# Performance work log

Hardware: AMD Instinct MI355X
Metric: run time of the kernel (lower is better)

Reference implementation:

```python
import jax, jax.numpy as jnp
import numpy as np

EMBED = 1024
D_MODEL = 1024
HEADS = 16
HEAD_DIM = D_MODEL // HEADS


def setup_inputs() -> dict:
    key = jax.random.key(0)
    ks = jax.random.split(key, 9)
    s = 1.0 / np.sqrt(EMBED)
    inp = {
        "x": jax.random.normal(ks[0], (4, 2048, EMBED), dtype=jnp.float32),
        "Wq": jax.random.uniform(ks[1], (EMBED, D_MODEL), jnp.float32, -s, s),
        "bq": jax.random.uniform(ks[2], (D_MODEL,), jnp.float32, -s, s),
        "Wk": jax.random.uniform(ks[3], (EMBED, D_MODEL), jnp.float32, -s, s),
        "bk": jax.random.uniform(ks[4], (D_MODEL,), jnp.float32, -s, s),
        "Wv": jax.random.uniform(ks[5], (EMBED, D_MODEL), jnp.float32, -s, s),
        "bv": jax.random.uniform(ks[6], (D_MODEL,), jnp.float32, -s, s),
        "Wo": jax.random.uniform(ks[7], (D_MODEL, D_MODEL), jnp.float32, -s, s),
        "bo": jax.random.uniform(ks[8], (D_MODEL,), jnp.float32, -s, s),
    }
    return inp


def reference(x, Wq, bq, Wk, bk, Wv, bv, Wo, bo):
    B, S, _ = x.shape
    # projections -> [B, H, S, Dh]
    def proj(W, b):
        return (x @ W + b).reshape(B, S, HEADS, HEAD_DIM).transpose(0, 2, 1, 3)
    q = proj(Wq, bq)
    k = proj(Wk, bk)
    v = proj(Wv, bv)
    energy = jnp.einsum("bhqd,bhkd->bhqk", q, k)  # [B,H,S,S]
    attn = jax.nn.softmax(energy / jnp.sqrt(jnp.float32(HEAD_DIM)), axis=-1)
    out = jnp.einsum("bhqk,bhkd->bhqd", attn, v)
    out = out.transpose(0, 2, 1, 3).reshape(B, S, D_MODEL)
    return out @ Wo + bo
```

## Files before the change

### kernel.cpp

```cpp
#include <hip/hip_runtime.h>

typedef unsigned short u16;
typedef unsigned int u32;
typedef unsigned short u16x8 __attribute__((ext_vector_type(8)));
typedef short s16x4 __attribute__((ext_vector_type(4)));
typedef __bf16 bf16x8 __attribute__((ext_vector_type(8)));
typedef float f32x4 __attribute__((ext_vector_type(4)));

#define QSCALE 0.18033688011112042f

__device__ __forceinline__ u16 f2bf(float f) {
    unsigned u = __float_as_uint(f);
    u += 0x7fffu + ((u >> 16) & 1u);
    return (u16)(u >> 16);
}

__device__ __forceinline__ bf16x8 ldfrag(const u16* p) {
    return __builtin_bit_cast(bf16x8, *(const u16x8*)p);
}

__device__ __forceinline__ void async_cp16(const void* g, void* l) {
    __builtin_amdgcn_global_load_lds(
        (const __attribute__((address_space(1))) unsigned int*)g,
        (__attribute__((address_space(3))) unsigned int*)l, 16, 0, 0);
}

__device__ __forceinline__ uint2 pack4(float a, float b, float c, float d) {
    uint2 w;
    w.x = (u32)f2bf(a) | ((u32)f2bf(b) << 16);
    w.y = (u32)f2bf(c) | ((u32)f2bf(d) << 16);
    return w;
}

__device__ __forceinline__ f32x4 mfma16(uint2 a, uint2 b, f32x4 c) {
#if __has_builtin(__builtin_amdgcn_mfma_f32_16x16x16bf16_1k)
    return __builtin_amdgcn_mfma_f32_16x16x16bf16_1k(
        __builtin_bit_cast(s16x4, a), __builtin_bit_cast(s16x4, b), c, 0, 0, 0);
#else
    asm volatile("s_nop 1\n\tv_mfma_f32_16x16x16_bf16 %0, %1, %2, %0"
                 : "+v"(c) : "v"(a), "v"(b));
    return c;
#endif
}


__global__ void cvt_x(const float* __restrict__ x, u16* __restrict__ xb, int n4) {
    int i = blockIdx.x * blockDim.x + threadIdx.x;
    if (i < n4) {
        float4 v = ((const float4*)x)[i];
        ushort4 o;
        o.x = f2bf(v.x); o.y = f2bf(v.y); o.z = f2bf(v.z); o.w = f2bf(v.w);
        ((ushort4*)xb)[i] = o;
    }
}

__global__ __launch_bounds__(1024) void transp(const float* __restrict__ src, u16* __restrict__ dst) {
    __shared__ float t[32][33];
    int bx = blockIdx.x * 32, by = blockIdx.y * 32;
    t[threadIdx.y][threadIdx.x] = src[(by + threadIdx.y) * 1024 + bx + threadIdx.x];
    __syncthreads();
    dst[(bx + threadIdx.y) * 1024 + by + threadIdx.x] = f2bf(t[threadIdx.x][threadIdx.y]);
}

__global__ void mkbias(const float* __restrict__ bq, const float* __restrict__ bk,
                       const float* __restrict__ bv, float* __restrict__ bqkv) {
    int i = blockIdx.x * blockDim.x + threadIdx.x;
    if (i < 3072) bqkv[i] = (i < 1024) ? bq[i] : (i < 2048 ? bk[i - 1024] : bv[i - 2048]);
}


template <int EPI>
__global__ __launch_bounds__(256)
void gemm128(const u16* __restrict__ A, const u16* __restrict__ Bt,
             const float* __restrict__ bias,
             u16* __restrict__ Qb, u16* __restrict__ Kb, u16* __restrict__ Vt,
             float* __restrict__ outf) {
    __shared__ u16 Asm[128 * 64];
    __shared__ u16 Bsm[128 * 64];
    int tid = threadIdx.x;
    int wave = tid >> 6, lane = tid & 63;
    int lr = lane & 15, lq = lane >> 4;
    int wrow = (wave >> 1) * 64, wcol = (wave & 1) * 64;
    int tileM = blockIdx.y * 128, tileN = blockIdx.x * 128;

    f32x4 acc[4][4];
    for (int i = 0; i < 4; i++)
        for (int j = 0; j < 4; j++)
            acc[i][j] = (f32x4){0.f, 0.f, 0.f, 0.f};

    int srow = tid >> 3;
    int sg = (tid & 7) ^ (srow & 7);
    const u16* ga = A + (tileM + srow) * 1024 + sg * 8;
    const u16* gb = Bt + (tileN + srow) * 1024 + sg * 8;
    u16* la = &Asm[tid * 8];
    u16* lb = &Bsm[tid * 8];

    int sw0 = ((lq ^ (lr & 7)) << 3);
    int sw1 = (((4 + lq) ^ (lr & 7)) << 3);

    for (int k0 = 0; k0 < 1024; k0 += 64) {
        for (int rnd = 0; rnd < 4; rnd++) {
            async_cp16(ga + k0 + rnd * 32 * 1024, la + rnd * 2048);
            async_cp16(gb + k0 + rnd * 32 * 1024, lb + rnd * 2048);
        }
        __syncthreads();
        for (int ko = 0; ko < 2; ko++) {
            int sw = ko ? sw1 : sw0;
            bf16x8 af[4], bfr[4];
            for (int mt = 0; mt < 4; mt++) af[mt] = ldfrag(&Asm[(wrow + mt * 16 + lr) * 64 + sw]);
            for (int nt = 0; nt < 4; nt++) bfr[nt] = ldfrag(&Bsm[(wcol + nt * 16 + lr) * 64 + sw]);
            for (int mt = 0; mt < 4; mt++)
                for (int nt = 0; nt < 4; nt++) {
                    if (EPI == 1)
                        acc[mt][nt] = __builtin_amdgcn_mfma_f32_16x16x32_bf16(af[mt], bfr[nt], acc[mt][nt], 0, 0, 0);
                    else
                        acc[mt][nt] = __builtin_amdgcn_mfma_f32_16x16x32_bf16(bfr[nt], af[mt], acc[mt][nt], 0, 0, 0);
                }
        }
        __syncthreads();
    }

    if (EPI == 0) {
        for (int mt = 0; mt < 4; mt++) {
            int m = tileM + wrow + mt * 16 + lr;
            int b = m >> 11, s = m & 2047;
            for (int nt = 0; nt < 4; nt++) {
                int n0 = tileN + wcol + nt * 16 + lq * 4;
                float4 bn = *(const float4*)&bias[n0];
                int which = n0 >> 10, d = n0 & 1023, h = d >> 6, dh = d & 63;
                u16* dst = (which ? Kb : Qb) + ((b * 16 + h) * 2048 + s) * 64 + dh;
                f32x4 v = acc[mt][nt];
                uint2 w;
                if (which == 0)
                    w = pack4((v[0] + bn.x) * QSCALE, (v[1] + bn.y) * QSCALE,
                              (v[2] + bn.z) * QSCALE, (v[3] + bn.w) * QSCALE);
                else
                    w = pack4(v[0] + bn.x, v[1] + bn.y, v[2] + bn.z, v[3] + bn.w);
                *(uint2*)dst = w;
            }
        }
    } else if (EPI == 1) {
        for (int nt = 0; nt < 4; nt++) {
            int n0 = tileN + wcol + nt * 16 + lr;
            float bn = bias[n0];
            int h = n0 >> 6, dh = n0 & 63;
            for (int mt = 0; mt < 4; mt++) {
                int m0 = tileM + wrow + mt * 16 + lq * 4;
                int b = m0 >> 11, s = m0 & 2047;
                f32x4 v = acc[mt][nt];
                uint2 w = pack4(v[0] + bn, v[1] + bn, v[2] + bn, v[3] + bn);
                *(uint2*)(Vt + ((b * 16 + h) * 64 + dh) * 2048 + s) = w;
            }
        }
    } else {
        for (int mt = 0; mt < 4; mt++) {
            int m = tileM + wrow + mt * 16 + lr;
            for (int nt = 0; nt < 4; nt++) {
                int n0 = tileN + wcol + nt * 16 + lq * 4;
                float4 bn = *(const float4*)&bias[n0];
                f32x4 v = acc[mt][nt];
                float4 st = {v[0] + bn.x, v[1] + bn.y, v[2] + bn.z, v[3] + bn.w};
                *(float4*)&outf[m * 1024 + n0] = st;
            }
        }
    }
}

__global__ __launch_bounds__(256)
void attn(const u16* __restrict__ Qb, const u16* __restrict__ Kb,
          const u16* __restrict__ Vt, u16* __restrict__ Ob) {
    __shared__ u16 Ksm[2][64 * 64];
    __shared__ u16 Vsm[2][64 * 64];
    int tid = threadIdx.x;
    int wave = tid >> 6, lane = tid & 63;
    int lr = lane & 15, lq = lane >> 4;
    int bh = blockIdx.y;
    int b = bh >> 4, h = bh & 15;
    int qbase = blockIdx.x * 128 + wave * 32;

    const u16* Qh = Qb + bh * 2048 * 64;
    const u16* Kh = Kb + bh * 2048 * 64;
    const u16* Vh = Vt + bh * 64 * 2048;

    bf16x8 qf[2][2];
    for (int s = 0; s < 2; s++)
        for (int hf = 0; hf < 2; hf++)
            qf[s][hf] = ldfrag(Qh + (qbase + s * 16 + lr) * 64 + hf * 32 + lq * 8);

    f32x4 o[2][4];
    float lacc[2] = {0.f, 0.f};
    for (int s = 0; s < 2; s++)
        for (int dt = 0; dt < 4; dt++) o[s][dt] = (f32x4){0.f, 0.f, 0.f, 0.f};

    int sw0 = (lq ^ (lr & 7)) << 3;

    int sr = tid >> 3, sg = tid & 7;
    int ksw = ((sg ^ (sr & 7)) << 3);
    const u16* gk = Kh + sr * 64 + ksw;
    const u16* gv = Vh + sr * 2048 + ksw;

    int vsub = (lq & 1) * 4;
    int vx = (lq >> 1);

    async_cp16(gk, &Ksm[0][tid * 8]);
    async_cp16(gk + 32 * 64, &Ksm[0][tid * 8 + 32 * 64]);
    async_cp16(gv, &Vsm[0][tid * 8]);
    async_cp16(gv + 32 * 2048, &Vsm[0][tid * 8 + 32 * 64]);

    for (int it = 0; it < 32; ++it) {
        int p = it & 1;
        __syncthreads();

        if (it < 31) {
            gk += 64 * 64; gv += 64;
            async_cp16(gk, &Ksm[p ^ 1][tid * 8]);
            async_cp16(gk + 32 * 64, &Ksm[p ^ 1][tid * 8 + 32 * 64]);
            async_cp16(gv, &Vsm[p ^ 1][tid * 8]);
            async_cp16(gv + 32 * 2048, &Vsm[p ^ 1][tid * 8 + 32 * 64]);
        }

        uint2 pb[2][4];
        for (int kg = 0; kg < 4; kg++) {
            const u16* krow = &Ksm[p][(kg * 16 + lr) * 64];
            bf16x8 kf0 = ldfrag(krow + sw0);
            bf16x8 kf1 = ldfrag(krow + (sw0 ^ 32));
            for (int s = 0; s < 2; s++) {
                f32x4 a = (f32x4){0.f, 0.f, 0.f, 0.f};
                a = __builtin_amdgcn_mfma_f32_16x16x32_bf16(kf0, qf[s][0], a, 0, 0, 0);
                a = __builtin_amdgcn_mfma_f32_16x16x32_bf16(kf1, qf[s][1], a, 0, 0, 0);
                float e0 = __builtin_amdgcn_exp2f(a[0]);
                float e1 = __builtin_amdgcn_exp2f(a[1]);
                float e2 = __builtin_amdgcn_exp2f(a[2]);
                float e3 = __builtin_amdgcn_exp2f(a[3]);
                lacc[s] += (e0 + e1) + (e2 + e3);
                pb[s][kg] = pack4(e0, e1, e2, e3);
            }
        }

        for (int kg = 0; kg < 4; kg++) {
            int vofs = (((2 * kg + vx) ^ (lr & 7)) << 3) + vsub;
            for (int dt = 0; dt < 4; dt++) {
                uint2 vf = *(const uint2*)&Vsm[p][(dt * 16 + lr) * 64 + vofs];
                o[0][dt] = mfma16(vf, pb[0][kg], o[0][dt]);
                o[1][dt] = mfma16(vf, pb[1][kg], o[1][dt]);
            }
        }
    }

    for (int s = 0; s < 2; s++) {
        lacc[s] += __shfl_xor(lacc[s], 16);
        lacc[s] += __shfl_xor(lacc[s], 32);
    }

    for (int s = 0; s < 2; s++) {
        float linv = 1.0f / lacc[s];
        int q = qbase + s * 16 + lr;
        u16* obase = Ob + (b * 2048 + q) * 1024 + h * 64 + lq * 4;
        for (int dt = 0; dt < 4; dt++) {
            uint2 w = pack4(o[s][dt][0] * linv, o[s][dt][1] * linv,
                            o[s][dt][2] * linv, o[s][dt][3] * linv);
            *(uint2*)(obase + dt * 16) = w;
        }
    }
}


extern "C" void kernel_launch(void* const* d_in, const int* in_sizes, int n_in,
                              void* d_out, int out_size, void* d_ws, size_t ws_size,
                              hipStream_t stream) {
    const float* x  = (const float*)d_in[0];
    const float* Wq = (const float*)d_in[1];
    const float* bq = (const float*)d_in[2];
    const float* Wk = (const float*)d_in[3];
    const float* bk = (const float*)d_in[4];
    const float* Wv = (const float*)d_in[5];
    const float* bv = (const float*)d_in[6];
    const float* Wo = (const float*)d_in[7];
    const float* bo = (const float*)d_in[8];
    float* out = (float*)d_out;

    char* ws = (char*)d_ws;
    u16* xb    = (u16*)ws;
    u16* Wt    = (u16*)(ws + (16u << 20));
    u16* Wot   = (u16*)(ws + (22u << 20));
    float* bqkv = (float*)(ws + (24u << 20));
    u16* Vtb   = (u16*)(ws + (25u << 20));
    u16* Qb    = (u16*)d_out;
    u16* Kb    = Qb + 4 * 16 * 2048 * 64;

    cvt_x<<<8192, 256, 0, stream>>>(x, xb, 8192 * 1024 / 4);
    dim3 tb(32, 32);
    transp<<<dim3(32, 32), tb, 0, stream>>>(Wq, Wt);
    transp<<<dim3(32, 32), tb, 0, stream>>>(Wk, Wt + 1024 * 1024);
    transp<<<dim3(32, 32), tb, 0, stream>>>(Wv, Wt + 2 * 1024 * 1024);
    transp<<<dim3(32, 32), tb, 0, stream>>>(Wo, Wot);
    mkbias<<<12, 256, 0, stream>>>(bq, bk, bv, bqkv);

    gemm128<0><<<dim3(16, 64), 256, 0, stream>>>(xb, Wt, bqkv, Qb, Kb, nullptr, nullptr);
    gemm128<1><<<dim3(8, 64), 256, 0, stream>>>(xb, Wt + 2048 * 1024, bqkv + 2048,
                                                nullptr, nullptr, Vtb, nullptr);
    attn<<<dim3(16, 64), 256, 0, stream>>>(Qb, Kb, Vtb, xb);
    gemm128<2><<<dim3(8, 64), 256, 0, stream>>>(xb, Wot, bo, nullptr, nullptr, nullptr, out);
}
```

Before: 327.7 us.

## Use 16x16x32 MFMA for PV product with permuted K rows and packed bf16 convert

Replaces the 16x16x16 bf16 MFMA used for the P·V product with the wider 16x16x32 instruction. K rows are permuted in shared memory so that each lane's exp'd scores form a contiguous 8-element bf16 fragment usable directly as the B operand. Score packing now uses the hardware v_cvt_pk_bf16_f32 instruction instead of software rounding. The aim is to halve the PV MFMA issue count, use wider LDS reads for V, and cut conversion ALU work, at the cost of a more intricate swizzle that must match between the global-load and read sides.

```diff
diff --git a/kernel.cpp b/kernel.cpp
--- a/kernel.cpp
+++ b/kernel.cpp
@@ -3,7 +3,7 @@
 typedef unsigned short u16;
 typedef unsigned int u32;
 typedef unsigned short u16x8 __attribute__((ext_vector_type(8)));
-typedef short s16x4 __attribute__((ext_vector_type(4)));
+typedef unsigned int u32x4 __attribute__((ext_vector_type(4)));
 typedef __bf16 bf16x8 __attribute__((ext_vector_type(8)));
 typedef float f32x4 __attribute__((ext_vector_type(4)));
 
@@ -13,6 +13,12 @@
     unsigned u = __float_as_uint(f);
     u += 0x7fffu + ((u >> 16) & 1u);
     return (u16)(u >> 16);
+}
+
+__device__ __forceinline__ u32 cvtpk(float lo, float hi) {
+    u32 r;
+    asm("v_cvt_pk_bf16_f32 %0, %1, %2" : "=v"(r) : "v"(lo), "v"(hi));
+    return r;
 }
 
 __device__ __forceinline__ bf16x8 ldfrag(const u16* p) {
@@ -32,15 +38,8 @@
     return w;
 }
 
-__device__ __forceinline__ f32x4 mfma16(uint2 a, uint2 b, f32x4 c) {
-#if __has_builtin(__builtin_amdgcn_mfma_f32_16x16x16bf16_1k)
-    return __builtin_amdgcn_mfma_f32_16x16x16bf16_1k(
-        __builtin_bit_cast(s16x4, a), __builtin_bit_cast(s16x4, b), c, 0, 0, 0);
-#else
-    asm volatile("s_nop 1\n\tv_mfma_f32_16x16x16_bf16 %0, %1, %2, %0"
-                 : "+v"(c) : "v"(a), "v"(b));
-    return c;
-#endif
+__device__ __forceinline__ f32x4 mfma32(bf16x8 a, bf16x8 b, f32x4 c) {
+    return __builtin_amdgcn_mfma_f32_16x16x32_bf16(a, b, c, 0, 0, 0);
 }
 
 
@@ -192,15 +191,16 @@
     for (int s = 0; s < 2; s++)
         for (int dt = 0; dt < 4; dt++) o[s][dt] = (f32x4){0.f, 0.f, 0.f, 0.f};
 
-    int sw0 = (lq ^ (lr & 7)) << 3;
+    int row0 = ((lr & 12) << 1) | (lr & 3);
+    int gg = (lr & 3) | (((lr >> 2) & 1) << 2);
+    int kofs = row0 * 64 + ((lq ^ gg) << 3);
+    int vofs0 = (lq ^ (lr & 7)) << 3;
 
     int sr = tid >> 3, sg = tid & 7;
-    int ksw = ((sg ^ (sr & 7)) << 3);
-    const u16* gk = Kh + sr * 64 + ksw;
-    const u16* gv = Vh + sr * 2048 + ksw;
-
-    int vsub = (lq & 1) * 4;
-    int vx = (lq >> 1);
+    int gK = (sg ^ ((sr & 3) | (((sr >> 3) & 1) << 2))) << 3;
+    int gV = (sg ^ (sr & 7)) << 3;
+    const u16* gk = Kh + sr * 64 + gK;
+    const u16* gv = Vh + sr * 2048 + gV;
 
     async_cp16(gk, &Ksm[0][tid * 8]);
     async_cp16(gk + 32 * 64, &Ksm[0][tid * 8 + 32 * 64]);
@@ -219,31 +219,45 @@
             async_cp16(gv + 32 * 2048, &Vsm[p ^ 1][tid * 8 + 32 * 64]);
         }
 
-        uint2 pb[2][4];
-        for (int kg = 0; kg < 4; kg++) {
-            const u16* krow = &Ksm[p][(kg * 16 + lr) * 64];
-            bf16x8 kf0 = ldfrag(krow + sw0);
-            bf16x8 kf1 = ldfrag(krow + (sw0 ^ 32));
+        const u16* Kp = Ksm[p];
+        const u16* Vp = Vsm[p];
+
+        bf16x8 pb[2][2];
+        for (int kg2 = 0; kg2 < 2; kg2++) {
+            int ka = kofs + kg2 * 2048;
+            bf16x8 kA0 = ldfrag(Kp + ka);
+            bf16x8 kA1 = ldfrag(Kp + (ka ^ 32));
+            bf16x8 kB0 = ldfrag(Kp + ka + 256);
+            bf16x8 kB1 = ldfrag(Kp + ((ka + 256) ^ 32));
             for (int s = 0; s < 2; s++) {
-                f32x4 a = (f32x4){0.f, 0.f, 0.f, 0.f};
-                a = __builtin_amdgcn_mfma_f32_16x16x32_bf16(kf0, qf[s][0], a, 0, 0, 0);
-                a = __builtin_amdgcn_mfma_f32_16x16x32_bf16(kf1, qf[s][1], a, 0, 0, 0);
-                float e0 = __builtin_amdgcn_exp2f(a[0]);
-                float e1 = __builtin_amdgcn_exp2f(a[1]);
-                float e2 = __builtin_amdgcn_exp2f(a[2]);
-                float e3 = __builtin_amdgcn_exp2f(a[3]);
-                lacc[s] += (e0 + e1) + (e2 + e3);
-                pb[s][kg] = pack4(e0, e1, e2, e3);
+                f32x4 sa = (f32x4){0.f, 0.f, 0.f, 0.f};
+                f32x4 sb = (f32x4){0.f, 0.f, 0.f, 0.f};
+                sa = mfma32(kA0, qf[s][0], sa);
+                sa = mfma32(kA1, qf[s][1], sa);
+                sb = mfma32(kB0, qf[s][0], sb);
+                sb = mfma32(kB1, qf[s][1], sb);
+                float e0 = __builtin_amdgcn_exp2f(sa[0]);
+                float e1 = __builtin_amdgcn_exp2f(sa[1]);
+                float e2 = __builtin_amdgcn_exp2f(sa[2]);
+                float e3 = __builtin_amdgcn_exp2f(sa[3]);
+                float e4 = __builtin_amdgcn_exp2f(sb[0]);
+                float e5 = __builtin_amdgcn_exp2f(sb[1]);
+                float e6 = __builtin_amdgcn_exp2f(sb[2]);
+                float e7 = __builtin_amdgcn_exp2f(sb[3]);
+                lacc[s] += ((e0 + e1) + (e2 + e3)) + ((e4 + e5) + (e6 + e7));
+                u32x4 pw = {cvtpk(e0, e1), cvtpk(e2, e3), cvtpk(e4, e5), cvtpk(e6, e7)};
+                pb[kg2][s] = __builtin_bit_cast(bf16x8, pw);
             }
         }
 
-        for (int kg = 0; kg < 4; kg++) {
-            int vofs = (((2 * kg + vx) ^ (lr & 7)) << 3) + vsub;
-            for (int dt = 0; dt < 4; dt++) {
-                uint2 vf = *(const uint2*)&Vsm[p][(dt * 16 + lr) * 64 + vofs];
-                o[0][dt] = mfma16(vf, pb[0][kg], o[0][dt]);
-                o[1][dt] = mfma16(vf, pb[1][kg], o[1][dt]);
-            }
+        for (int dt = 0; dt < 4; dt++) {
+            int rb = (dt * 16 + lr) * 64;
+            bf16x8 v0 = ldfrag(Vp + rb + vofs0);
+            bf16x8 v1 = ldfrag(Vp + rb + (vofs0 ^ 32));
+            o[0][dt] = mfma32(v0, pb[0][0], o[0][dt]);
+            o[1][dt] = mfma32(v0, pb[0][1], o[1][dt]);
+            o[0][dt] = mfma32(v1, pb[1][0], o[0][dt]);
+            o[1][dt] = mfma32(v1, pb[1][1], o[1][dt]);
         }
     }
 
```

Result: faster. 307.4 us (-6.2%).
